# Kernel tuning notes

Measured on AMD Instinct MI355X. Metric: run time of the kernel, lower is better.

Reference implementation:

```python
import jax, jax.numpy as jnp
import numpy as np

T = 5
EPS = 1e-05


def setup_inputs() -> dict:
    key = jax.random.key(0)
    X = jax.random.normal(key, (64, 512, 32, 32), dtype=jnp.float32)
    return {"X": X}


def reference(X):
    # IterNorm (training branch): whiten channels via Newton-Schulz inverse sqrt.
    N, C, H, W = X.shape
    x = jnp.transpose(X, (1, 0, 2, 3)).reshape(C, -1)  # [d, m], d=C, m=N*H*W
    d, m = x.shape
    mean = jnp.mean(x, axis=-1, keepdims=True)
    xc = x - mean
    I = jnp.eye(d, dtype=X.dtype)
    # Sigma = eps*I + (1/m) xc xc^T  (addmm(eps, I, 1/m, xc, xc^T))
    Sigma = EPS * I + (xc @ xc.T) / m
    rTr = 1.0 / jnp.trace(Sigma)          # (Sigma * I).sum().reciprocal()
    Sigma_N = Sigma * rTr
    P = I
    for _ in range(T):
        # P_{k+1} = 1.5*P_k - 0.5 * P_k^3 @ Sigma_N
        P = 1.5 * P - 0.5 * (P @ P @ P) @ Sigma_N
    wm = P * jnp.sqrt(rTr)                # whitening matrix ~ Sigma^{-1/2}
    xn = wm @ xc                          # [d, m]
    Xn = jnp.transpose(xn.reshape(C, N, H, W), (1, 0, 2, 3))
    return Xn
```

## Files before the change

### kernel.cpp

```cpp
#include <hip/hip_runtime.h>
#include <math.h>

#define Nn   64
#define Cc   512
#define HWs  1024
#define CHW  (Cc * HWs)
#define Mm   (Nn * HWs)
#define EPSC 1e-5f
#define NBC  64

typedef unsigned int   u32;
typedef unsigned short u16;
typedef __attribute__((ext_vector_type(8))) short  short8;
typedef __attribute__((ext_vector_type(4))) float  floatx4;

__device__ __forceinline__ u16 f2bf(float f) {
    u32 u = __float_as_uint(f);
    u += 0x7fff + ((u >> 16) & 1);
    return (u16)(u >> 16);
}
__device__ __forceinline__ float bf2f(u16 h) {
    return __uint_as_float(((u32)h) << 16);
}

__device__ __forceinline__ void gld_lds16(const u16* g, u16* l) {
    __builtin_amdgcn_global_load_lds(
        (const __attribute__((address_space(1))) u32*)g,
        (__attribute__((address_space(3))) u32*)l, 16, 0, 0);
}

__global__ __launch_bounds__(256) void convert_transpose(const float* __restrict__ X,
                                                         u16* __restrict__ Xbf,
                                                         u16* __restrict__ Xt,
                                                         float* __restrict__ meanP) {
    const int hT = blockIdx.x;
    const int h0 = hT << 6;
    const int c0 = blockIdx.y << 6;
    const int n  = blockIdx.z;
    const int t  = threadIdx.x;
    __shared__ u16   T[64][65];
    __shared__ float red[64][17];

    const float* Xn  = X   + (size_t)n * CHW;
    u16*         Xbn = Xbf + (size_t)n * CHW;
    u16*         Xtn = Xt  + (size_t)n * CHW;

    const int cl = t >> 4;
    const int h4 = (t & 15) << 2;
#pragma unroll
    for (int i = 0; i < 4; ++i) {
        const int c = cl + (i << 4);
        float4 v = *(const float4*)&Xn[(size_t)(c0 + c) * HWs + h0 + h4];
        red[c][t & 15] = v.x + v.y + v.z + v.w;
        u16 b0 = f2bf(v.x), b1 = f2bf(v.y), b2 = f2bf(v.z), b3 = f2bf(v.w);
        *(ushort4*)&Xbn[(size_t)(c0 + c) * HWs + h0 + h4] = make_ushort4(b0, b1, b2, b3);
        T[c][h4]     = b0;
        T[c][h4 + 1] = b1;
        T[c][h4 + 2] = b2;
        T[c][h4 + 3] = b3;
    }
    __syncthreads();
    const int hl = t >> 4;
    const int c4 = (t & 15) << 2;
#pragma unroll
    for (int i = 0; i < 4; ++i) {
        const int h = hl + (i << 4);
        ushort4 pk = make_ushort4(T[c4][h], T[c4 + 1][h], T[c4 + 2][h], T[c4 + 3][h]);
        *(ushort4*)&Xtn[(size_t)(h0 + h) * Cc + c0 + c4] = pk;
    }
    if (t < 64) {
        float s = 0.f;
#pragma unroll
        for (int j = 0; j < 16; ++j) s += red[t][j];
        atomicAdd(&meanP[hT * 512 + c0 + t], s);
    }
}

__global__ __launch_bounds__(256) void gram_mfma(const u16* __restrict__ Xbf,
                                                 float* __restrict__ G) {
    static const int TI[10] = {0,0,0,0,1,1,1,2,2,3};
    static const int TJ[10] = {0,1,2,3,1,2,3,2,3,3};
    const int id = blockIdx.x;
    const int q  = id >> 3;
    const int x  = q % 10;
    const int y  = (id & 7) + ((q / 10) << 3);
    const int i0 = TI[x] << 7;
    const int j0 = TJ[x] << 7;
    const int n0 = y << 1;
    const int t  = threadIdx.x;
    const int w  = t >> 6, l = t & 63;

    __shared__ u16 As[128 * 32];
    __shared__ u16 Bs[128 * 32];

    floatx4 acc[4][4];
#pragma unroll
    for (int mi = 0; mi < 4; ++mi)
#pragma unroll
        for (int ni = 0; ni < 4; ++ni) acc[mi][ni] = (floatx4){0.f, 0.f, 0.f, 0.f};

    const int lr = l >> 2;
    const int lc = (l & 3) << 3;
    const int wm = w >> 1, wn = w & 1;
    const int fm = l & 15, fq = l >> 4;

    for (int n = n0; n < n0 + 2; ++n) {
        const u16* Xn = Xbf + (size_t)n * CHW;
        for (int hw = 0; hw < HWs; hw += 32) {
#pragma unroll
            for (int p = 0; p < 2; ++p) {
                const int g   = w * 2 + p;
                const int row = g * 16 + lr;
                gld_lds16(Xn + (size_t)(i0 + row) * HWs + hw + lc, &As[g * 512]);
                gld_lds16(Xn + (size_t)(j0 + row) * HWs + hw + lc, &Bs[g * 512]);
            }
            __syncthreads();
            short8 a[4], b[4];
#pragma unroll
            for (int mi = 0; mi < 4; ++mi)
                a[mi] = *(const short8*)&As[(wm * 64 + mi * 16 + fm) * 32 + fq * 8];
#pragma unroll
            for (int ni = 0; ni < 4; ++ni)
                b[ni] = *(const short8*)&Bs[(wn * 64 + ni * 16 + fm) * 32 + fq * 8];
#pragma unroll
            for (int mi = 0; mi < 4; ++mi)
#pragma unroll
                for (int ni = 0; ni < 4; ++ni)
                    acc[mi][ni] = __builtin_amdgcn_mfma_f32_16x16x32_bf16(
                        a[mi], b[ni], acc[mi][ni], 0, 0, 0);
            __syncthreads();
        }
    }
#pragma unroll
    for (int mi = 0; mi < 4; ++mi)
#pragma unroll
        for (int ni = 0; ni < 4; ++ni)
#pragma unroll
            for (int r = 0; r < 4; ++r) {
                const int gi = i0 + wm * 64 + mi * 16 + fq * 4 + r;
                const int gj = j0 + wn * 64 + ni * 16 + fm;
                atomicAdd(&G[(size_t)gi * Cc + gj], acc[mi][ni][r]);
            }
}

__device__ __forceinline__ void gridbar(int* bar, int gen) {
    __syncthreads();
    if (threadIdx.x == 0) {
        __threadfence();
        __hip_atomic_fetch_add(bar, 1, __ATOMIC_RELEASE, __HIP_MEMORY_SCOPE_AGENT);
        while (__hip_atomic_load(bar, __ATOMIC_ACQUIRE, __HIP_MEMORY_SCOPE_AGENT) < gen * NBC)
            __builtin_amdgcn_s_sleep(1);
        __threadfence();
    }
    __syncthreads();
}

__device__ void mm_phase(const u16* Ah, const u16* Al, const u16* Bh, const u16* Bl,
                         float alpha, const float* D, float beta,
                         float* Cf, u16* Ch, u16* Cl, u16* S) {
    const int bid = blockIdx.x;
    const int i0 = (bid >> 3) << 6, j0 = (bid & 7) << 6;
    const int t = threadIdx.x, w = t >> 6, l = t & 63;
    const int wm = w >> 1, wn = w & 1, fm = l & 15, fq = l >> 4;
    const u16* src = (w == 0) ? Ah : (w == 1) ? Al : (w == 2) ? Bh : Bl;
    const int rbase = (w < 2) ? i0 : j0;
    u16* myl = S + (w << 12);
    const int srow = l >> 3;
    const int skb  = ((l & 7) ^ srow) << 3;
    const int f7   = fm & 7;

    floatx4 acc[2][2];
#pragma unroll
    for (int mi = 0; mi < 2; ++mi)
#pragma unroll
        for (int ni = 0; ni < 2; ++ni) acc[mi][ni] = (floatx4){0.f, 0.f, 0.f, 0.f};

    for (int k0 = 0; k0 < 512; k0 += 64) {
#pragma unroll
        for (int g = 0; g < 8; ++g)
            gld_lds16(src + (size_t)(rbase + (g << 3) + srow) * 512 + k0 + skb,
                      myl + (g << 9));
        __syncthreads();
#pragma unroll
        for (int kc = 0; kc < 2; ++kc) {
            short8 ah[2], al[2], bh[2], bl[2];
            const int kq = ((kc << 2) + fq);
#pragma unroll
            for (int mi = 0; mi < 2; ++mi) {
                const int r   = wm * 32 + mi * 16 + fm;
                const int off = (r << 6) + ((kq ^ f7) << 3);
                ah[mi] = *(const short8*)&S[off];
                al[mi] = *(const short8*)&S[4096 + off];
            }
#pragma unroll
            for (int ni = 0; ni < 2; ++ni) {
                const int r   = wn * 32 + ni * 16 + fm;
                const int off = (r << 6) + ((kq ^ f7) << 3);
                bh[ni] = *(const short8*)&S[8192 + off];
                bl[ni] = *(const short8*)&S[12288 + off];
            }
#pragma unroll
            for (int mi = 0; mi < 2; ++mi)
#pragma unroll
                for (int ni = 0; ni < 2; ++ni) {
                    acc[mi][ni] = __builtin_amdgcn_mfma_f32_16x16x32_bf16(ah[mi], bh[ni], acc[mi][ni], 0, 0, 0);
                    acc[mi][ni] = __builtin_amdgcn_mfma_f32_16x16x32_bf16(ah[mi], bl[ni], acc[mi][ni], 0, 0, 0);
                    acc[mi][ni] = __builtin_amdgcn_mfma_f32_16x16x32_bf16(al[mi], bh[ni], acc[mi][ni], 0, 0, 0);
                }
        }
        __syncthreads();
    }

#pragma unroll
    for (int mi = 0; mi < 2; ++mi)
#pragma unroll
        for (int ni = 0; ni < 2; ++ni)
#pragma unroll
            for (int r4 = 0; r4 < 4; ++r4) {
                const int gi = i0 + wm * 32 + mi * 16 + fq * 4 + r4;
                const int gj = j0 + wn * 32 + ni * 16 + fm;
                const size_t idx = (size_t)gi * 512 + gj;
                float v = alpha * acc[mi][ni][r4];
                if (D) v += beta * D[idx];
                if (Cf) Cf[idx] = v;
                const u16 h = f2bf(v);
                Ch[idx] = h;
                Cl[idx] = f2bf(v - bf2f(h));
            }
}

__global__ __launch_bounds__(256) void ns_chain(
    const float* G, const float* meanP, float* scal, int* bar,
    float* mean, float* wmmv,
    u16* Sh, u16* Sl, u16* PhA, u16* PlA, u16* PhB, u16* PlB,
    u16* T2h, u16* T2l, u16* T3h, u16* T3l, float* PfA, float* PfB) {
    __shared__ u16 S[4 * 4096];
    const int t = threadIdx.x, b = blockIdx.x;

    {
        const int c = b * 8 + (t >> 5);
        const int q = t & 31;
        float s = (q < 16) ? meanP[(size_t)q * 512 + c] : 0.f;
#pragma unroll
        for (int o = 16; o > 0; o >>= 1) s += __shfl_xor(s, o);
        if (q == 0) {
            const float mc = s * (1.0f / Mm);
            mean[c] = mc;
            const float tc = G[(size_t)c * 513] * (1.0f / Mm) - mc * mc;
            atomicAdd(&scal[2], tc);
        }
    }
    gridbar(bar, 1);
    if (b == 0 && t == 0) {
        const float tr  = scal[2] + (float)Cc * EPSC;
        const float rtr = 1.0f / tr;
        scal[0] = rtr;
        scal[1] = sqrtf(rtr);
    }
    gridbar(bar, 2);

    {
        const float rtr = scal[0];
#pragma unroll
        for (int k2 = 0; k2 < 16; ++k2) {
            const int e = (b << 12) + (k2 << 8) + t;
            const int i = e >> 9, j = e & 511;
            const float g = (i <= j) ? G[((size_t)i << 9) + j] : G[((size_t)j << 9) + i];
            float sig = g * (1.0f / Mm) - mean[i] * mean[j];
            if (i == j) sig += EPSC;
            const float sN = sig * rtr;
            const u16 sh = f2bf(sN);
            Sh[e] = sh;
            Sl[e] = f2bf(sN - bf2f(sh));
            const float p1 = ((i == j) ? 1.5f : 0.f) - 0.5f * sN;
            PfA[e] = p1;
            const u16 ph = f2bf(p1);
            PhA[e] = ph;
            PlA[e] = f2bf(p1 - bf2f(ph));
        }
    }
    gridbar(bar, 3);

    int gen = 3;
    u16 *ph = PhA, *pl = PlA, *qh = PhB, *ql = PlB;
    float *pf = PfA, *qf = PfB;
    for (int it = 0; it < 4; ++it) {
        mm_phase(ph, pl, ph, pl, 1.f, nullptr, 0.f, nullptr, T2h, T2l, S);
        gridbar(bar, ++gen);
        mm_phase(T2h, T2l, ph, pl, 1.f, nullptr, 0.f, nullptr, T3h, T3l, S);
        gridbar(bar, ++gen);
        mm_phase(T3h, T3l, Sh, Sl, -0.5f, pf, 1.5f, qf, qh, ql, S);
        gridbar(bar, ++gen);
        { u16* x = ph; ph = qh; qh = x; }
        { u16* x = pl; pl = ql; ql = x; }
        { float* x = pf; pf = qf; qf = x; }
    }

    {
        const int c = b * 8 + (t >> 5);
        const int q = t & 31;
        float s = 0.f;
#pragma unroll
        for (int k2 = 0; k2 < 16; ++k2) {
            const int j = q + (k2 << 5);
            s += pf[((size_t)c << 9) + j] * mean[j];
        }
#pragma unroll
        for (int o = 16; o > 0; o >>= 1) s += __shfl_xor(s, o);
        if (q == 0) wmmv[c] = s * scal[1];
    }
}

__global__ __launch_bounds__(256) void whiten_mfma(const u16* __restrict__ Xt,
                                                   const u16* __restrict__ Pbf,
                                                   const float* __restrict__ wmm,
                                                   const float* __restrict__ scal,
                                                   float* __restrict__ out) {
    const int id  = blockIdx.x;
    const int m   = (id >> 3) & 3;
    const int grp = (id & 7) + ((id >> 5) << 3);
    const int c0  = m << 7;
    const int h0  = (grp & 7) << 7;
    const int n   = grp >> 3;
    const int t   = threadIdx.x;
    const int w   = t >> 6, l = t & 63;

    __shared__ char smem[128 * 68 * 4];
    u16* As = (u16*)smem;
    u16* Bs = As + 4096;
    float* Ep = (float*)smem;

    floatx4 acc[4][4];
#pragma unroll
    for (int mi = 0; mi < 4; ++mi)
#pragma unroll
        for (int ni = 0; ni < 4; ++ni) acc[mi][ni] = (floatx4){0.f, 0.f, 0.f, 0.f};

    const int lr = l >> 2;
    const int lc = (l & 3) << 3;
    const int wm = w >> 1, wn = w & 1;
    const int fm = l & 15, fq = l >> 4;

    const u16* Xn = Xt + (size_t)n * CHW;

    for (int kk = 0; kk < Cc; kk += 32) {
#pragma unroll
        for (int p = 0; p < 2; ++p) {
            const int g   = w * 2 + p;
            const int row = g * 16 + lr;
            gld_lds16(Xn  + (size_t)(h0 + row) * Cc + kk + lc, &As[g * 512]);
            gld_lds16(Pbf + (size_t)(c0 + row) * Cc + kk + lc, &Bs[g * 512]);
        }
        __syncthreads();
        short8 a[4], b[4];
#pragma unroll
        for (int mi = 0; mi < 4; ++mi)
            a[mi] = *(const short8*)&As[(wm * 64 + mi * 16 + fm) * 32 + fq * 8];
#pragma unroll
        for (int ni = 0; ni < 4; ++ni)
            b[ni] = *(const short8*)&Bs[(wn * 64 + ni * 16 + fm) * 32 + fq * 8];
#pragma unroll
        for (int mi = 0; mi < 4; ++mi)
#pragma unroll
            for (int ni = 0; ni < 4; ++ni)
                acc[mi][ni] = __builtin_amdgcn_mfma_f32_16x16x32_bf16(
                    a[mi], b[ni], acc[mi][ni], 0, 0, 0);
        __syncthreads();
    }

    const float sr = scal[1];
    float wv[4];
#pragma unroll
    for (int ni = 0; ni < 4; ++ni) wv[ni] = wmm[c0 + wn * 64 + ni * 16 + fm];
    float* outn = out + (size_t)n * CHW;

#pragma unroll
    for (int mp = 0; mp < 2; ++mp) {
        __syncthreads();
#pragma unroll
        for (int p = 0; p < 2; ++p) {
            const int mi = mp * 2 + p;
#pragma unroll
            for (int ni = 0; ni < 4; ++ni) {
                const int row  = wn * 64 + ni * 16 + fm;
                const int slot = wm * 32 + p * 16 + fq * 4;
                floatx4 v = acc[mi][ni] * sr - wv[ni];
                *(floatx4*)&Ep[row * 68 + slot] = v;
            }
        }
        __syncthreads();
#pragma unroll
        for (int jj = 0; jj < 8; ++jj) {
            const int idx = jj * 256 + t;
            const int row = idx >> 4;
            const int s4  = (idx & 15) << 2;
            const int wmr = s4 >> 5;
            const int within = s4 & 31;
            float4 v = *(const float4*)&Ep[row * 68 + s4];
            *(float4*)&outn[(size_t)(c0 + row) * HWs + h0 + wmr * 64 + mp * 32 + within] = v;
        }
    }
}

__global__ __launch_bounds__(256) void mean_kernel(const float* __restrict__ X,
                                                   float* __restrict__ mean) {
    const int c = blockIdx.x;
    const int t = threadIdx.x;
    float s = 0.f;
    for (int n = 0; n < Nn; ++n) {
        const float4* p = (const float4*)(X + (size_t)n * CHW + (size_t)c * HWs);
        float4 v = p[t];
        s += v.x + v.y + v.z + v.w;
    }
    __shared__ float red[256];
    red[t] = s;
    __syncthreads();
    for (int o = 128; o > 0; o >>= 1) {
        if (t < o) red[t] += red[t + o];
        __syncthreads();
    }
    if (t == 0) mean[c] = red[0] * (1.0f / Mm);
}

__global__ __launch_bounds__(256) void trace_fb(const float* __restrict__ G,
                                                const float* __restrict__ mean,
                                                float* __restrict__ scal) {
    const int t = threadIdx.x;
    float s = 0.f;
    for (int i = t; i < Cc; i += 256)
        s += G[(size_t)i * Cc + i] * (1.0f / Mm) - mean[i] * mean[i];
    __shared__ float red[256];
    red[t] = s;
    __syncthreads();
    for (int o = 128; o > 0; o >>= 1) {
        if (t < o) red[t] += red[t + o];
        __syncthreads();
    }
    if (t == 0) {
        const float tr  = red[0] + (float)Cc * EPSC;
        const float rtr = 1.0f / tr;
        scal[0] = rtr;
        scal[1] = sqrtf(rtr);
    }
}

__global__ __launch_bounds__(256) void gram_kernel(const float* __restrict__ X,
                                                   float* __restrict__ G) {
    const int ti = blockIdx.x >> 3, tj = blockIdx.x & 7;
    const int i0 = ti << 6, j0 = tj << 6;
    const int n0 = blockIdx.y << 3;
    const int t  = threadIdx.x;
    const int tx = t & 15, ty = t >> 4;
    __shared__ float As[64][33];
    __shared__ float Bs[64][33];
    float acc[4][4] = {};
    const int lc = t & 31;
    const int lr0 = t >> 5;
    for (int n = n0; n < n0 + 8; ++n) {
        const float* Xn = X + (size_t)n * CHW;
        for (int hw0 = 0; hw0 < HWs; hw0 += 32) {
#pragma unroll
            for (int r = 0; r < 8; ++r) {
                const int row = lr0 + (r << 3);
                As[row][lc] = Xn[(size_t)(i0 + row) * HWs + hw0 + lc];
                Bs[row][lc] = Xn[(size_t)(j0 + row) * HWs + hw0 + lc];
            }
            __syncthreads();
#pragma unroll
            for (int k = 0; k < 32; ++k) {
                float a[4], b[4];
#pragma unroll
                for (int r = 0; r < 4; ++r) a[r] = As[(ty << 2) + r][k];
#pragma unroll
                for (int cn = 0; cn < 4; ++cn) b[cn] = Bs[(tx << 2) + cn][k];
#pragma unroll
                for (int r = 0; r < 4; ++r)
#pragma unroll
                    for (int cn = 0; cn < 4; ++cn) acc[r][cn] += a[r] * b[cn];
            }
            __syncthreads();
        }
    }
#pragma unroll
    for (int r = 0; r < 4; ++r)
#pragma unroll
        for (int cn = 0; cn < 4; ++cn)
            atomicAdd(&G[(size_t)(i0 + (ty << 2) + r) * Cc + j0 + (tx << 2) + cn],
                      acc[r][cn]);
}

__global__ __launch_bounds__(256) void sigman_full_kernel(const float* __restrict__ G,
                                                          const float* __restrict__ mean,
                                                          const float* __restrict__ scal,
                                                          float* __restrict__ S,
                                                          float* __restrict__ P) {
    const int e = blockIdx.x * 256 + threadIdx.x;
    const int i = e >> 9, j = e & 511;
    const float rtr = scal[0];
    float sig = G[e] * (1.0f / Mm) - mean[i] * mean[j];
    if (i == j) sig += EPSC;
    S[e] = sig * rtr;
    P[e] = (i == j) ? 1.f : 0.f;
}

__global__ __launch_bounds__(256) void mm512_kernel(const float* __restrict__ A,
                                                    const float* __restrict__ B,
                                                    float* __restrict__ C,
                                                    float alpha,
                                                    const float* __restrict__ D,
                                                    float beta) {
    const int ti = blockIdx.x >> 3, tj = blockIdx.x & 7;
    const int i0 = ti << 6, j0 = tj << 6;
    const int t  = threadIdx.x;
    const int tx = t & 15, ty = t >> 4;
    __shared__ float As[64][33];
    __shared__ float Bs[32][65];
    float acc[4][4] = {};
    const int lcA = t & 31, lrA = t >> 5;
    const int lcB = t & 63, lrB = t >> 6;
    for (int k0 = 0; k0 < 512; k0 += 32) {
#pragma unroll
        for (int r = 0; r < 8; ++r) {
            const int row = lrA + (r << 3);
            As[row][lcA] = A[(size_t)(i0 + row) * 512 + k0 + lcA];
        }
#pragma unroll
        for (int r = 0; r < 8; ++r) {
            const int row = lrB + (r << 2);
            Bs[row][lcB] = B[(size_t)(k0 + row) * 512 + j0 + lcB];
        }
        __syncthreads();
#pragma unroll
        for (int k = 0; k < 32; ++k) {
            float a[4], b[4];
#pragma unroll
            for (int r = 0; r < 4; ++r) a[r] = As[(ty << 2) + r][k];
#pragma unroll
            for (int cn = 0; cn < 4; ++cn) b[cn] = Bs[k][(tx << 2) + cn];
#pragma unroll
            for (int r = 0; r < 4; ++r)
#pragma unroll
                for (int cn = 0; cn < 4; ++cn) acc[r][cn] += a[r] * b[cn];
        }
        __syncthreads();
    }
#pragma unroll
    for (int r = 0; r < 4; ++r) {
        const size_t idx = (size_t)(i0 + (ty << 2) + r) * 512 + j0 + (tx << 2);
        float4 v;
        v.x = alpha * acc[r][0];
        v.y = alpha * acc[r][1];
        v.z = alpha * acc[r][2];
        v.w = alpha * acc[r][3];
        if (D) {
            const float4 d = *(const float4*)(D + idx);
            v.x += beta * d.x; v.y += beta * d.y; v.z += beta * d.z; v.w += beta * d.w;
        }
        *(float4*)(C + idx) = v;
    }
}

__global__ __launch_bounds__(128) void wmm_kernel(const float* __restrict__ P,
                                                  const float* __restrict__ mean,
                                                  const float* __restrict__ scal,
                                                  float* __restrict__ wmm) {
    const int c = blockIdx.x, t = threadIdx.x;
    float s = 0.f;
    for (int j = t; j < Cc; j += 128) s += P[(size_t)c * Cc + j] * mean[j];
    __shared__ float red[128];
    red[t] = s;
    __syncthreads();
    for (int o = 64; o > 0; o >>= 1) {
        if (t < o) red[t] += red[t + o];
        __syncthreads();
    }
    if (t == 0) wmm[c] = red[0] * scal[1];
}

__global__ __launch_bounds__(256) void whiten_kernel(const float* __restrict__ X,
                                                     const float* __restrict__ P,
                                                     const float* __restrict__ wmm,
                                                     const float* __restrict__ scal,
                                                     float* __restrict__ out) {
    const int c0 = blockIdx.x << 6;
    const int h0 = blockIdx.y << 6;
    const int n  = blockIdx.z;
    const int t  = threadIdx.x;
    const int tx = t & 15, ty = t >> 4;
    __shared__ float Ps[64][33];
    __shared__ float Xs[32][65];
    float acc[4][4] = {};
    const int lcA = t & 31, lrA = t >> 5;
    const int lcB = t & 63, lrB = t >> 6;
    const float* Xn = X + (size_t)n * CHW;
    for (int k0 = 0; k0 < 512; k0 += 32) {
#pragma unroll
        for (int r = 0; r < 8; ++r) {
            const int row = lrA + (r << 3);
            Ps[row][lcA] = P[(size_t)(c0 + row) * 512 + k0 + lcA];
        }
#pragma unroll
        for (int r = 0; r < 8; ++r) {
            const int row = lrB + (r << 2);
            Xs[row][lcB] = Xn[(size_t)(k0 + row) * HWs + h0 + lcB];
        }
        __syncthreads();
#pragma unroll
        for (int k = 0; k < 32; ++k) {
            float a[4], b[4];
#pragma unroll
            for (int r = 0; r < 4; ++r) a[r] = Ps[(ty << 2) + r][k];
#pragma unroll
            for (int cn = 0; cn < 4; ++cn) b[cn] = Xs[k][(tx << 2) + cn];
#pragma unroll
            for (int r = 0; r < 4; ++r)
#pragma unroll
                for (int cn = 0; cn < 4; ++cn) acc[r][cn] += a[r] * b[cn];
        }
        __syncthreads();
    }
    const float sr = scal[1];
#pragma unroll
    for (int r = 0; r < 4; ++r) {
        const int c = c0 + (ty << 2) + r;
        const float wv = wmm[c];
        float4 v;
        v.x = sr * acc[r][0] - wv;
        v.y = sr * acc[r][1] - wv;
        v.z = sr * acc[r][2] - wv;
        v.w = sr * acc[r][3] - wv;
        *(float4*)(out + (size_t)n * CHW + (size_t)c * HWs + h0 + (tx << 2)) = v;
    }
}

extern "C" void kernel_launch(void* const* d_in, const int* in_sizes, int n_in,
                              void* d_out, int out_size, void* d_ws, size_t ws_size,
                              hipStream_t stream) {
    const float* X = (const float*)d_in[0];
    float* out     = (float*)d_out;

    const size_t NU16 = 33554432;
    const size_t NM   = 262144;
    const size_t NEED = NU16 * 2 * 2
                      + NM * 10 * 2
                      + (NM + 8192 + 32 + 512 + 512 + 2 * NM) * 4;

    if (ws_size >= NEED) {
        u16* Xbf = (u16*)d_ws;
        u16* Xt  = Xbf + NU16;
        u16* Sh  = Xt  + NU16;
        u16* Sl  = Sh + NM;
        u16* PhA = Sl + NM;
        u16* PlA = PhA + NM;
        u16* PhB = PlA + NM;
        u16* PlB = PhB + NM;
        u16* T2h = PlB + NM;
        u16* T2l = T2h + NM;
        u16* T3h = T2l + NM;
        u16* T3l = T3h + NM;
        float* G     = (float*)(T3l + NM);
        float* meanP = G + NM;
        float* scal  = meanP + 8192;
        int*   bar   = (int*)(scal + 16);
        float* mean  = (float*)(bar + 16);
        float* wmm   = mean + 512;
        float* PfA   = wmm + 512;
        float* PfB   = PfA + NM;

        hipMemsetAsync(G, 0, (NM + 8192 + 32) * sizeof(float), stream);
        convert_transpose<<<dim3(16, 8, 64), 256, 0, stream>>>(X, Xbf, Xt, meanP);
        gram_mfma<<<320, 256, 0, stream>>>(Xbf, G);
        ns_chain<<<NBC, 256, 0, stream>>>(G, meanP, scal, bar, mean, wmm,
                                          Sh, Sl, PhA, PlA, PhB, PlB,
                                          T2h, T2l, T3h, T3l, PfA, PfB);
        whiten_mfma<<<2048, 256, 0, stream>>>(Xt, PhA, wmm, scal, out);
    } else {
        float* ws   = (float*)d_ws;
        float* mean = ws;
        float* wmm  = ws + 512;
        float* scal = ws + 1024;
        float* G    = ws + 2048;
        float* S    = G + 262144;
        float* Pa   = S + 262144;
        float* Pb   = Pa + 262144;
        float* P2   = Pb + 262144;
        float* P3   = P2 + 262144;

        mean_kernel<<<512, 256, 0, stream>>>(X, mean);
        hipMemsetAsync(G, 0, sizeof(float) * 262144, stream);
        gram_kernel<<<dim3(64, 8), 256, 0, stream>>>(X, G);
        trace_fb<<<1, 256, 0, stream>>>(G, mean, scal);
        sigman_full_kernel<<<1024, 256, 0, stream>>>(G, mean, scal, S, Pa);

        float* P  = Pa;
        float* Pn = Pb;
        for (int it = 0; it < 5; ++it) {
            mm512_kernel<<<64, 256, 0, stream>>>(P, P, P2, 1.f, nullptr, 0.f);
            mm512_kernel<<<64, 256, 0, stream>>>(P2, P, P3, 1.f, nullptr, 0.f);
            mm512_kernel<<<64, 256, 0, stream>>>(P3, S, Pn, -0.5f, P, 1.5f);
            float* tmp = P; P = Pn; Pn = tmp;
        }

        wmm_kernel<<<512, 128, 0, stream>>>(P, mean, scal, wmm);
        whiten_kernel<<<dim3(8, 16, 64), 256, 0, stream>>>(X, P, wmm, scal, out);
    }
}
```

Before: 547.8 us.

## Reassociate Newton-Schulz step to compute P² and P·Σ concurrently

Each iteration now computes P·P on 64 blocks while 64 more blocks compute P·Σ_N in parallel, then forms P²·(P·Σ_N). This cuts the per-iteration dependent matmul phases and grid barriers from three to two, relying on P commuting with Σ_N because P is a polynomial in it. Every block now redundantly computes the channel means and trace into LDS, which removes two initial grid barriers. The panel matmul stages the full K dimension into a larger LDS buffer in two batches instead of eight small loads, trading occupancy and LDS space for fewer block syncs.

New measurement: 579.3 us. 1.06x slower.

```diff
diff --git a/kernel.cpp b/kernel.cpp
--- a/kernel.cpp
+++ b/kernel.cpp
@@ -7,7 +7,7 @@
 #define CHW  (Cc * HWs)
 #define Mm   (Nn * HWs)
 #define EPSC 1e-5f
-#define NBC  64
+#define NBC  128
 
 typedef unsigned int   u32;
 typedef unsigned short u16;
@@ -155,19 +155,16 @@
     __syncthreads();
 }
 
-__device__ void mm_phase(const u16* Ah, const u16* Al, const u16* Bh, const u16* Bl,
-                         float alpha, const float* D, float beta,
-                         float* Cf, u16* Ch, u16* Cl, u16* S) {
-    const int bid = blockIdx.x;
-    const int i0 = (bid >> 3) << 6, j0 = (bid & 7) << 6;
+__device__ __forceinline__ void mm_panel(const u16* Ah, const u16* Al,
+                                         const u16* Bh, const u16* Bl,
+                                         int i0, int j0,
+                                         float alpha, const float* D, float beta,
+                                         float* Cf, u16* Ch, u16* Cl, u16* S) {
     const int t = threadIdx.x, w = t >> 6, l = t & 63;
     const int wm = w >> 1, wn = w & 1, fm = l & 15, fq = l >> 4;
     const u16* src = (w == 0) ? Ah : (w == 1) ? Al : (w == 2) ? Bh : Bl;
     const int rbase = (w < 2) ? i0 : j0;
-    u16* myl = S + (w << 12);
-    const int srow = l >> 3;
-    const int skb  = ((l & 7) ^ srow) << 3;
-    const int f7   = fm & 7;
+    const int lr = l >> 2, lc = (l & 3) << 3;
 
     floatx4 acc[2][2];
 #pragma unroll
@@ -175,29 +172,32 @@
 #pragma unroll
         for (int ni = 0; ni < 2; ++ni) acc[mi][ni] = (floatx4){0.f, 0.f, 0.f, 0.f};
 
-    for (int k0 = 0; k0 < 512; k0 += 64) {
-#pragma unroll
-        for (int g = 0; g < 8; ++g)
-            gld_lds16(src + (size_t)(rbase + (g << 3) + srow) * 512 + k0 + skb,
-                      myl + (g << 9));
-        __syncthreads();
-#pragma unroll
-        for (int kc = 0; kc < 2; ++kc) {
+    auto issue = [&](int cc, int bb) {
+        u16* dst = S + bb * 32768 + w * 8192;
+        const u16* sp = src + (size_t)rbase * 512 + cc * 128;
+#pragma unroll
+        for (int s = 0; s < 4; ++s)
+#pragma unroll
+            for (int g = 0; g < 4; ++g)
+                gld_lds16(sp + (size_t)(g * 16 + lr) * 512 + s * 32 + lc,
+                          dst + s * 2048 + g * 512);
+    };
+    auto compute = [&](int bb) {
+        const u16* base = S + bb * 32768;
+#pragma unroll
+        for (int s = 0; s < 4; ++s) {
             short8 ah[2], al[2], bh[2], bl[2];
-            const int kq = ((kc << 2) + fq);
 #pragma unroll
             for (int mi = 0; mi < 2; ++mi) {
-                const int r   = wm * 32 + mi * 16 + fm;
-                const int off = (r << 6) + ((kq ^ f7) << 3);
-                ah[mi] = *(const short8*)&S[off];
-                al[mi] = *(const short8*)&S[4096 + off];
+                const int ro = s * 2048 + (wm * 32 + mi * 16 + fm) * 32 + fq * 8;
+                ah[mi] = *(const short8*)&base[ro];
+                al[mi] = *(const short8*)&base[8192 + ro];
             }
 #pragma unroll
             for (int ni = 0; ni < 2; ++ni) {
-                const int r   = wn * 32 + ni * 16 + fm;
-                const int off = (r << 6) + ((kq ^ f7) << 3);
-                bh[ni] = *(const short8*)&S[8192 + off];
-                bl[ni] = *(const short8*)&S[12288 + off];
+                const int ro = s * 2048 + (wn * 32 + ni * 16 + fm) * 32 + fq * 8;
+                bh[ni] = *(const short8*)&base[16384 + ro];
+                bl[ni] = *(const short8*)&base[24576 + ro];
             }
 #pragma unroll
             for (int mi = 0; mi < 2; ++mi)
@@ -208,8 +208,17 @@
                     acc[mi][ni] = __builtin_amdgcn_mfma_f32_16x16x32_bf16(al[mi], bh[ni], acc[mi][ni], 0, 0, 0);
                 }
         }
-        __syncthreads();
-    }
+    };
+
+    issue(0, 0); issue(1, 1);
+    __syncthreads();
+    compute(0);
+    compute(1);
+    __syncthreads();
+    issue(2, 0); issue(3, 1);
+    __syncthreads();
+    compute(0);
+    compute(1);
 
 #pragma unroll
     for (int mi = 0; mi < 2; ++mi)
@@ -230,66 +239,69 @@
 }
 
 __global__ __launch_bounds__(256) void ns_chain(
-    const float* G, const float* meanP, float* scal, int* bar,
-    float* mean, float* wmmv,
+    const float* G, const float* meanP, float* scal, int* bar, float* wmmv,
     u16* Sh, u16* Sl, u16* PhA, u16* PlA, u16* PhB, u16* PlB,
-    u16* T2h, u16* T2l, u16* T3h, u16* T3l, float* PfA, float* PfB) {
-    __shared__ u16 S[4 * 4096];
+    u16* T2h, u16* T2l, u16* Wh, u16* Wl, float* PfA, float* PfB) {
+    __shared__ u16   S[65536];
+    __shared__ float meanL[512];
+    __shared__ float redL[4];
     const int t = threadIdx.x, b = blockIdx.x;
-
-    {
-        const int c = b * 8 + (t >> 5);
-        const int q = t & 31;
-        float s = (q < 16) ? meanP[(size_t)q * 512 + c] : 0.f;
-#pragma unroll
-        for (int o = 16; o > 0; o >>= 1) s += __shfl_xor(s, o);
-        if (q == 0) {
-            const float mc = s * (1.0f / Mm);
-            mean[c] = mc;
-            const float tc = G[(size_t)c * 513] * (1.0f / Mm) - mc * mc;
-            atomicAdd(&scal[2], tc);
-        }
-    }
-    gridbar(bar, 1);
-    if (b == 0 && t == 0) {
-        const float tr  = scal[2] + (float)Cc * EPSC;
-        const float rtr = 1.0f / tr;
-        scal[0] = rtr;
-        scal[1] = sqrtf(rtr);
-    }
-    gridbar(bar, 2);
-
-    {
-        const float rtr = scal[0];
-#pragma unroll
-        for (int k2 = 0; k2 < 16; ++k2) {
-            const int e = (b << 12) + (k2 << 8) + t;
-            const int i = e >> 9, j = e & 511;
-            const float g = (i <= j) ? G[((size_t)i << 9) + j] : G[((size_t)j << 9) + i];
-            float sig = g * (1.0f / Mm) - mean[i] * mean[j];
-            if (i == j) sig += EPSC;
-            const float sN = sig * rtr;
-            const u16 sh = f2bf(sN);
-            Sh[e] = sh;
-            Sl[e] = f2bf(sN - bf2f(sh));
-            const float p1 = ((i == j) ? 1.5f : 0.f) - 0.5f * sN;
-            PfA[e] = p1;
-            const u16 ph = f2bf(p1);
-            PhA[e] = ph;
-            PlA[e] = f2bf(p1 - bf2f(ph));
-        }
-    }
-    gridbar(bar, 3);
-
-    int gen = 3;
+    const int w = t >> 6, l = t & 63;
+
+    float tp = 0.f;
+#pragma unroll
+    for (int cb = 0; cb < 2; ++cb) {
+        const int c = t + (cb << 8);
+        float s = 0.f;
+#pragma unroll
+        for (int q = 0; q < 16; ++q) s += meanP[(q << 9) + c];
+        const float mc = s * (1.0f / Mm);
+        meanL[c] = mc;
+        tp += G[(size_t)c * 513] * (1.0f / Mm) - mc * mc;
+    }
+#pragma unroll
+    for (int o = 32; o > 0; o >>= 1) tp += __shfl_xor(tp, o);
+    if (l == 0) redL[w] = tp;
+    __syncthreads();
+    const float tr  = redL[0] + redL[1] + redL[2] + redL[3] + (float)Cc * EPSC;
+    const float rtr = 1.0f / tr;
+    const float sr  = sqrtf(rtr);
+    if (b == 0 && t == 0) { scal[0] = rtr; scal[1] = sr; }
+
+#pragma unroll
+    for (int k2 = 0; k2 < 8; ++k2) {
+        const int e = (b << 11) + (k2 << 8) + t;
+        const int i = e >> 9, j = e & 511;
+        const float g = (i <= j) ? G[((size_t)i << 9) + j] : G[((size_t)j << 9) + i];
+        float sig = g * (1.0f / Mm) - meanL[i] * meanL[j];
+        if (i == j) sig += EPSC;
+        const float sN = sig * rtr;
+        const u16 sh = f2bf(sN);
+        Sh[e] = sh;
+        Sl[e] = f2bf(sN - bf2f(sh));
+        const float p1 = ((i == j) ? 1.5f : 0.f) - 0.5f * sN;
+        PfA[e] = p1;
+        const u16 ph = f2bf(p1);
+        PhA[e] = ph;
+        PlA[e] = f2bf(p1 - bf2f(ph));
+    }
+    int gen = 0;
+    gridbar(bar, ++gen);
+
     u16 *ph = PhA, *pl = PlA, *qh = PhB, *ql = PlB;
     float *pf = PfA, *qf = PfB;
+    const int i0 = ((b & 63) >> 3) << 6, j0 = (b & 7) << 6;
     for (int it = 0; it < 4; ++it) {
-        mm_phase(ph, pl, ph, pl, 1.f, nullptr, 0.f, nullptr, T2h, T2l, S);
+        if (b < 64)
+            mm_panel(ph, pl, ph, pl, i0, j0, 1.f, nullptr, 0.f,
+                     nullptr, T2h, T2l, S);
+        else
+            mm_panel(ph, pl, Sh, Sl, i0, j0, 1.f, nullptr, 0.f,
+                     nullptr, Wh, Wl, S);
         gridbar(bar, ++gen);
-        mm_phase(T2h, T2l, ph, pl, 1.f, nullptr, 0.f, nullptr, T3h, T3l, S);
-        gridbar(bar, ++gen);
-        mm_phase(T3h, T3l, Sh, Sl, -0.5f, pf, 1.5f, qf, qh, ql, S);
+        if (b < 64)
+            mm_panel(T2h, T2l, Wh, Wl, i0, j0, -0.5f, pf, 1.5f,
+                     qf, qh, ql, S);
         gridbar(bar, ++gen);
         { u16* x = ph; ph = qh; qh = x; }
         { u16* x = pl; pl = ql; ql = x; }
@@ -297,17 +309,16 @@
     }
 
     {
-        const int c = b * 8 + (t >> 5);
-        const int q = t & 31;
+        const int c = (b << 2) + (t >> 6);
         float s = 0.f;
 #pragma unroll
-        for (int k2 = 0; k2 < 16; ++k2) {
-            const int j = q + (k2 << 5);
-            s += pf[((size_t)c << 9) + j] * mean[j];
-        }
-#pragma unroll
-        for (int o = 16; o > 0; o >>= 1) s += __shfl_xor(s, o);
-        if (q == 0) wmmv[c] = s * scal[1];
+        for (int jj = 0; jj < 8; ++jj) {
+            const int j = l + (jj << 6);
+            s += pf[((size_t)c << 9) + j] * meanL[j];
+        }
+#pragma unroll
+        for (int o = 32; o > 0; o >>= 1) s += __shfl_xor(s, o);
+        if (l == 0) wmmv[c] = s * sr;
     }
 }
 
@@ -656,9 +667,9 @@
         u16* PlB = PhB + NM;
         u16* T2h = PlB + NM;
         u16* T2l = T2h + NM;
-        u16* T3h = T2l + NM;
-        u16* T3l = T3h + NM;
-        float* G     = (float*)(T3l + NM);
+        u16* Wh  = T2l + NM;
+        u16* Wl  = Wh + NM;
+        float* G     = (float*)(Wl + NM);
         float* meanP = G + NM;
         float* scal  = meanP + 8192;
         int*   bar   = (int*)(scal + 16);
@@ -670,9 +681,9 @@
         hipMemsetAsync(G, 0, (NM + 8192 + 32) * sizeof(float), stream);
         convert_transpose<<<dim3(16, 8, 64), 256, 0, stream>>>(X, Xbf, Xt, meanP);
         gram_mfma<<<320, 256, 0, stream>>>(Xbf, G);
-        ns_chain<<<NBC, 256, 0, stream>>>(G, meanP, scal, bar, mean, wmm,
+        ns_chain<<<NBC, 256, 0, stream>>>(G, meanP, scal, bar, wmm,
                                           Sh, Sl, PhA, PlA, PhB, PlB,
-                                          T2h, T2l, T3h, T3l, PfA, PfB);
+                                          T2h, T2l, Wh, Wl, PfA, PfB);
         whiten_mfma<<<2048, 256, 0, stream>>>(Xt, PhA, wmm, scal, out);
     } else {
         float* ws   = (float*)d_ws;
```
